# Optimization experiments

Hardware: AMD Instinct MI355X
Metric: run time of the kernel (lower is better)

Reference implementation:

```python
import jax, jax.numpy as jnp
import numpy as np

K = 9          # 3x3 deformable kernel positions
EPS = 1e-5     # BatchNorm eps


def conv3x3(x, w, stride=1):
    # x: [B,C,H,W], w: [O,I,3,3], padding=1
    return jax.lax.conv_general_dilated(
        x, w, (stride, stride), ((1, 1), (1, 1)),
        dimension_numbers=('NCHW', 'OIHW', 'NCHW'))


def _bilinear_sample(img, py, px):
    # img: [C,H,W]; py,px: [K,Ho,Wo] float sample coords (zero outside).
    H, W = img.shape[1], img.shape[2]
    y0 = jnp.floor(py)
    x0 = jnp.floor(px)

    def corner(yc, xc):
        w = (1.0 - jnp.abs(py - yc)) * (1.0 - jnp.abs(px - xc))
        valid = (yc >= 0) & (yc <= H - 1) & (xc >= 0) & (xc <= W - 1)
        yi = jnp.clip(yc, 0, H - 1).astype(jnp.int32)
        xi = jnp.clip(xc, 0, W - 1).astype(jnp.int32)
        v = img[:, yi, xi]                      # [C,K,Ho,Wo]
        return v * (w * valid)[None]

    return (corner(y0, x0) + corner(y0, x0 + 1) +
            corner(y0 + 1, x0) + corner(y0 + 1, x0 + 1))


def deform_conv2d(x, offset, mask, w, stride=1, pad=1):
    # x: [B,Cin,H,W]; offset: [B,2K,Ho,Wo] (y,x interleaved per tap);
    # mask: [B,K,Ho,Wo]; w: [Cout,Cin,3,3]. torchvision DCNv2 semantics.
    B, Cin = x.shape[0], x.shape[1]
    Ho, Wo = offset.shape[2], offset.shape[3]
    Cout = w.shape[0]
    kh, kw = jnp.meshgrid(jnp.arange(3), jnp.arange(3), indexing='ij')
    kh = kh.reshape(K).astype(x.dtype)
    kw = kw.reshape(K).astype(x.dtype)
    base_y = (jnp.arange(Ho) * stride - pad).astype(x.dtype)
    base_x = (jnp.arange(Wo) * stride - pad).astype(x.dtype)
    off = offset.reshape(B, K, 2, Ho, Wo)
    py = base_y[None, None, :, None] + kh[None, :, None, None] + off[:, :, 0]
    px = base_x[None, None, None, :] + kw[None, :, None, None] + off[:, :, 1]
    g = jax.vmap(_bilinear_sample)(x, py, px)     # [B,Cin,K,Ho,Wo]
    g = g * mask[:, None]
    return jnp.einsum('bikhw,oik->bohw', g, w.reshape(Cout, Cin, K))


def batchnorm(x, gamma, beta, mean, var):
    # eval-mode BN over channel dim of [B,C,H,W]
    inv = jax.lax.rsqrt(var + EPS) * gamma
    return x * inv[None, :, None, None] + (beta - mean * inv)[None, :, None, None]


def setup_inputs() -> dict:
    key = jax.random.key(0)
    ks = jax.random.split(key, 20)
    B, Cin, H, W = 16, 64, 64, 64
    C1, C2, NC = 128, 128, 1000
    inp = {
        'x': jax.random.normal(ks[0], (B, Cin, H, W), jnp.float32),
        'conv1_w': jax.random.normal(ks[1], (C1, Cin, 3, 3), jnp.float32) * 0.05,
        'off1_w': jax.random.normal(ks[2], (2 * K, Cin, 3, 3), jnp.float32) * 0.02,
        'mod1_w': jax.random.normal(ks[3], (K, Cin, 3, 3), jnp.float32) * 0.05,
        'bn1_g': jax.random.uniform(ks[4], (C1,), jnp.float32, 0.5, 1.5),
        'bn1_b': jax.random.normal(ks[5], (C1,), jnp.float32) * 0.1,
        'bn1_m': jax.random.normal(ks[6], (C1,), jnp.float32) * 0.1,
        'bn1_v': jax.random.uniform(ks[7], (C1,), jnp.float32, 0.5, 1.5),
        'conv2_w': jax.random.normal(ks[8], (C2, C1, 3, 3), jnp.float32) * 0.05,
        'off2_w': jax.random.normal(ks[9], (2 * K, C1, 3, 3), jnp.float32) * 0.02,
        'mod2_w': jax.random.normal(ks[10], (K, C1, 3, 3), jnp.float32) * 0.05,
        'bn2_g': jax.random.uniform(ks[11], (C2,), jnp.float32, 0.5, 1.5),
        'bn2_b': jax.random.normal(ks[12], (C2,), jnp.float32) * 0.1,
        'bn2_m': jax.random.normal(ks[13], (C2,), jnp.float32) * 0.1,
        'bn2_v': jax.random.uniform(ks[14], (C2,), jnp.float32, 0.5, 1.5),
        'fc_w': jax.random.normal(ks[15], (NC, C2), jnp.float32) * 0.05,
        'fc_b': jnp.zeros((NC,), jnp.float32),
    }
    return inp


def reference(x, conv1_w, off1_w, mod1_w, bn1_g, bn1_b, bn1_m, bn1_v,
              conv2_w, off2_w, mod2_w, bn2_g, bn2_b, bn2_m, bn2_v,
              fc_w, fc_b):
    stride = 1
    # stage 1: deformable conv (offset + sigmoid modulation) + BN + ReLU
    off = conv3x3(x, off1_w, stride)
    mask = jax.nn.sigmoid(conv3x3(x, mod1_w, stride))
    out = deform_conv2d(x, off, mask, conv1_w, stride=stride, pad=1)
    out = jax.nn.relu(batchnorm(out, bn1_g, bn1_b, bn1_m, bn1_v))
    # stage 2: deformable conv + BN (no ReLU before GAP, as in source)
    off = conv3x3(out, off2_w, stride)
    mask = jax.nn.sigmoid(conv3x3(out, mod2_w, stride))
    out = deform_conv2d(out, off, mask, conv2_w, stride=stride, pad=1)
    out = batchnorm(out, bn2_g, bn2_b, bn2_m, bn2_v)
    # global average pool + fc
    out = out.mean(axis=(2, 3))                 # [B, C2]
    return out @ fc_w.T + fc_b
```

## Files before the change

### kernel.cpp

```cpp
#include <hip/hip_runtime.h>

#define TPB 256
typedef unsigned short us;
typedef __attribute__((ext_vector_type(8))) _Float16 f16x8;
typedef __attribute__((ext_vector_type(2))) _Float16 f16x2;
typedef __attribute__((ext_vector_type(4))) float f32x4;

__device__ inline us f2h(float f){ union{ _Float16 h; us u; } x; x.h = (_Float16)f; return x.u; }
__device__ inline f16x2 u2h2(unsigned u){ union{ unsigned v; f16x2 h; } x; x.v = u; return x.h; }
#define MFMA16(a,b,c) __builtin_amdgcn_mfma_f32_16x16x32_f16((a),(b),(c),0,0,0)

__global__ __launch_bounds__(256) void k_transpose_x(const float* __restrict__ x,
                                                     us* __restrict__ xT){
  __shared__ float tile[64][65];
  const int y = blockIdx.x, b = blockIdx.y;
  for (int i = threadIdx.x; i < 4096; i += TPB){
    const int c = i >> 6, xx = i & 63;
    tile[c][xx] = x[b*262144 + c*4096 + y*64 + xx];
  }
  __syncthreads();
  for (int i = threadIdx.x; i < 4096; i += TPB){
    const int xx = i >> 6, c = i & 63;
    xT[(size_t)(b*4096 + y*64 + xx)*64 + c] = f2h(tile[c][xx]);
  }
}

__global__ __launch_bounds__(256) void k_prep(
    const float* __restrict__ cw1, const float* __restrict__ ow1, const float* __restrict__ mw1,
    const float* __restrict__ cw2, const float* __restrict__ ow2, const float* __restrict__ mw2,
    us* __restrict__ d1, us* __restrict__ d2, us* __restrict__ a1, us* __restrict__ a2){
  const int e = blockIdx.x*TPB + threadIdx.x;
  if (e < 73728){
    int k = e/8192, r = e%8192, kb = r/4096, r2 = r%4096;
    int n0 = r2>>9, q = r2&511, l = q>>3, j = q&7;
    int co = n0*16 + (l&15), c = kb*32 + (l>>4)*8 + j;
    d1[e] = f2h(cw1[(co*64 + c)*9 + k]);
  }
  if (e < 147456){
    int k = e/16384, r = e%16384, kb = r/4096, r2 = r%4096;
    int n0 = r2>>9, q = r2&511, l = q>>3, j = q&7;
    int co = n0*16 + (l&15), c = kb*32 + (l>>4)*8 + j;
    d2[e] = f2h(cw2[(co*128 + c)*9 + k]);
  }
  if (e < 18432){
    int k = e/2048, r = e%2048, kb = r/1024, r2 = r%1024;
    int n0 = r2>>9, q = r2&511, l = q>>3, j = q&7;
    int co = n0*16 + (l&15), c = kb*32 + (l>>4)*8 + j;
    float w = (co < 18) ? ow1[(co*64 + c)*9 + k] : (co < 27 ? mw1[((co-18)*64 + c)*9 + k] : 0.f);
    a1[e] = f2h(w);
  }
  if (e < 36864){
    int k = e/4096, r = e%4096, kb = r/1024, r2 = r%1024;
    int n0 = r2>>9, q = r2&511, l = q>>3, j = q&7;
    int co = n0*16 + (l&15), c = kb*32 + (l>>4)*8 + j;
    float w = (co < 18) ? ow2[(co*128 + c)*9 + k] : (co < 27 ? mw2[((co-18)*128 + c)*9 + k] : 0.f);
    a2[e] = f2h(w);
  }
}

template<int CIN, int STAGE>
__global__ __launch_bounds__(512, 4) void k_fused(
    const us* __restrict__ inT,
    const us* __restrict__ wb_aux, const us* __restrict__ wb_def,
    const float* __restrict__ bn_g, const float* __restrict__ bn_b,
    const float* __restrict__ bn_m, const float* __restrict__ bn_v,
    us* __restrict__ outT, float* __restrict__ partial){
  constexpr int KB2  = CIN/64;
  constexpr int NC   = 9*KB2;
  constexpr int WE_A = 2*(CIN/32)*512;
  constexpr int WE_D = 8*(CIN/32)*512;

  __shared__ __align__(16) us pool[12672];
  __shared__ uint4 otab[576];
  __shared__ uint2 wtab[576];
  __shared__ float extra[256];

  const int id  = blockIdx.x;
  const int nid = (id & 7)*128 + (id >> 3);
  const int b = nid >> 6, ho = nid & 63;
  const int tid = threadIdx.x;
  const us* __restrict__ inb = inT + (size_t)b*4096*CIN;
  const char* __restrict__ inbc = (const char*)inb;

  if (STAGE == 1 && tid < 128){
    float inv = rsqrtf(bn_v[tid] + 1e-5f)*bn_g[tid];
    extra[tid] = inv; extra[128 + tid] = bn_b[tid] - bn_m[tid]*inv;
  }

  const int lane = tid & 63, lr = lane & 15, lg = lane >> 4;
  const int wv = tid >> 6;

  const int mh = wv & 3, nh = wv >> 2;
  f32x4 aacc = (f32x4){0.f,0.f,0.f,0.f};
  for (int kb2 = 0; kb2 < KB2; ++kb2){
    if (kb2) __syncthreads();
    for (int s = tid; s < 1584; s += 512){
      const int slot = s >> 3, cq = s & 7;
      const int r = slot/66, p = slot - r*66;
      const int y = ho - 1 + r, x = p - 1;
      uint4 q = make_uint4(0u,0u,0u,0u);
      if (y >= 0 && y < 64 && x >= 0 && x < 64)
        q = *(const uint4*)(inb + (size_t)(y*64 + x)*CIN + kb2*64 + cq*8);
      *(uint4*)(pool + slot*64 + ((cq ^ (slot & 7))*8)) = q;
    }
    __syncthreads();
    #pragma unroll
    for (int k = 0; k < 9; ++k){
      const int kh = k/3, kw = k - kh*3;
      const int slot = kh*66 + mh*16 + lr + kw;
      #pragma unroll
      for (int kbl = 0; kbl < 2; ++kbl){
        f16x8 a = *(const f16x8*)(pool + slot*64 + (((kbl*4 + lg) ^ (slot & 7))*8));
        f16x8 bf = *(const f16x8*)(wb_aux + (size_t)k*WE_A + (size_t)((kb2*2 + kbl)*2 + nh)*512 + lane*8);
        aacc = MFMA16(a, bf, aacc);
      }
    }
  }
  __syncthreads();

  float* am = (float*)pool;
  {
    const int co = nh*16 + lr;
    if (co < 27){
      #pragma unroll
      for (int i = 0; i < 4; ++i) am[co*66 + mh*16 + lg*4 + i] = aacc[i];
    }
  }
  __syncthreads();

  for (int sid = tid; sid < 576; sid += 512){
    const int k = sid >> 6, px = sid & 63;
    const int kh = k/3, kw = k - kh*3;
    float oy = am[(2*k)*66 + px];
    float ox = am[(2*k+1)*66 + px];
    float mv = 1.f/(1.f + expf(-am[(18+k)*66 + px]));
    float py  = (float)(ho - 1 + kh) + oy;
    float pxx = (float)(px - 1 + kw) + ox;
    float fyf = floorf(py), fxf = floorf(pxx);
    int y0 = (int)fyf, x0 = (int)fxf;
    float dy = py - fyf, dx = pxx - fxf;
    bool vy0 = (y0 >= 0) && (y0 < 64), vy1 = (y0 >= -1) && (y0 < 63);
    bool vx0 = (x0 >= 0) && (x0 < 64), vx1 = (x0 >= -1) && (x0 < 63);
    int y0c = min(max(y0,0),63), y1c = min(max(y0+1,0),63);
    int x0c = min(max(x0,0),63), x1c = min(max(x0+1,0),63);
    const unsigned str = CIN*2u;
    otab[sid] = make_uint4((unsigned)(y0c*64 + x0c)*str, (unsigned)(y0c*64 + x1c)*str,
                           (unsigned)(y1c*64 + x0c)*str, (unsigned)(y1c*64 + x1c)*str);
    float w00 = (1.f-dy)*(1.f-dx)*mv*((vy0 && vx0) ? 1.f : 0.f);
    float w01 = (1.f-dy)*dx     *mv*((vy0 && vx1) ? 1.f : 0.f);
    float w10 = dy*(1.f-dx)     *mv*((vy1 && vx0) ? 1.f : 0.f);
    float w11 = dy*dx           *mv*((vy1 && vx1) ? 1.f : 0.f);
    wtab[sid] = make_uint2((unsigned)f2h(w00) | ((unsigned)f2h(w01) << 16),
                           (unsigned)f2h(w10) | ((unsigned)f2h(w11) << 16));
  }
  __syncthreads();

  f32x4 acc[4];
  #pragma unroll
  for (int m = 0; m < 4; ++m) acc[m] = (f32x4){0.f,0.f,0.f,0.f};

  const int pxs = tid >> 3, cqs = tid & 7;

  auto load_corners = [&](int i, f16x8* cr){
    const int k = i/KB2, kb2 = i - (i/KB2)*KB2;
    const uint4 o = otab[k*64 + pxs];
    const unsigned c0 = (unsigned)(kb2*64 + cqs*8)*2u;
    cr[0] = *(const f16x8*)(inbc + o.x + c0);
    cr[1] = *(const f16x8*)(inbc + o.y + c0);
    cr[2] = *(const f16x8*)(inbc + o.z + c0);
    cr[3] = *(const f16x8*)(inbc + o.w + c0);
  };
  auto load_B = [&](int i, f16x8* bbp){
    const int k = i/KB2, kb2 = i - (i/KB2)*KB2;
    #pragma unroll
    for (int kbl = 0; kbl < 2; ++kbl)
      bbp[kbl] = *(const f16x8*)(wb_def + (size_t)k*WE_D + (size_t)((kb2*2 + kbl)*8 + wv)*512 + lane*8);
  };
  auto blend_write = [&](int i, const f16x8* cr, us* dst){
    const int k = i/KB2;
    const uint2 wp = wtab[k*64 + pxs];
    const f16x2 wAB = u2h2(wp.x), wCD = u2h2(wp.y);
    const _Float16 wA = wAB[0], wB = wAB[1], wC = wCD[0], wD = wCD[1];
    const f16x8 va = (f16x8){wA,wA,wA,wA,wA,wA,wA,wA};
    const f16x8 vb = (f16x8){wB,wB,wB,wB,wB,wB,wB,wB};
    const f16x8 vc = (f16x8){wC,wC,wC,wC,wC,wC,wC,wC};
    const f16x8 vd = (f16x8){wD,wD,wD,wD,wD,wD,wD,wD};
    f16x8 r = cr[0]*va + cr[1]*vb;
    r = r + cr[2]*vc + cr[3]*vd;
    *(f16x8*)(dst + pxs*64 + ((cqs ^ (pxs & 7))*8)) = r;
  };
  auto mfma_def = [&](int i, const us* src, const f16x8* bbp){
    #pragma unroll
    for (int kbl = 0; kbl < 2; ++kbl){
      #pragma unroll
      for (int mt = 0; mt < 4; ++mt){
        const int row = mt*16 + lr;
        f16x8 a = *(const f16x8*)(src + row*64 + (((kbl*4 + lg) ^ (row & 7))*8));
        acc[mt] = MFMA16(a, bbp[kbl], acc[mt]);
      }
    }
  };

  us* g0 = pool;
  us* g1 = pool + 4096;
  f16x8 crn[4], bb[2], bbn[2];
  load_corners(0, crn);
  load_B(0, bb);
  blend_write(0, crn, g0);
  __syncthreads();
  for (int i = 0; i < NC; ++i){
    us* cur = (i & 1) ? g1 : g0;
    us* nxt = (i & 1) ? g0 : g1;
    const bool more = (i + 1 < NC);
    if (more){ load_corners(i+1, crn); load_B(i+1, bbn); }
    mfma_def(i, cur, bb);
    if (more) blend_write(i+1, crn, nxt);
    bb[0] = bbn[0]; bb[1] = bbn[1];
    __syncthreads();
  }

  if (STAGE == 1){
    const size_t rowbase = (size_t)(b*4096 + ho*64)*128;
    const int co = wv*16 + lr;
    const float inv = extra[co], bia = extra[128 + co];
    #pragma unroll
    for (int mt = 0; mt < 4; ++mt){
      const int pxl = mt*16 + lg*4;
      #pragma unroll
      for (int i = 0; i < 4; ++i){
        float v = acc[mt][i]*inv + bia;
        outT[rowbase + (size_t)(pxl + i)*128 + co] = f2h(fmaxf(v, 0.f));
      }
    }
  } else {
    float s = 0.f;
    #pragma unroll
    for (int mt = 0; mt < 4; ++mt)
      s += acc[mt][0] + acc[mt][1] + acc[mt][2] + acc[mt][3];
    s += __shfl_xor(s, 16);
    s += __shfl_xor(s, 32);
    if (lane < 16) extra[wv*16 + lane] = s;
    __syncthreads();
    if (tid < 128) partial[(size_t)(b*64 + ho)*128 + tid] = extra[tid];
  }
}

__global__ __launch_bounds__(256) void k_pool(
    const float* __restrict__ partial,
    const float* __restrict__ g2, const float* __restrict__ b2,
    const float* __restrict__ m2, const float* __restrict__ v2,
    float* __restrict__ pooled){
  const int t = blockIdx.x*TPB + threadIdx.x;
  if (t >= 2048) return;
  const int b = t >> 7, c = t & 127;
  float s = 0.f;
  for (int h = 0; h < 64; ++h) s += partial[(b*64 + h)*128 + c];
  const float inv = rsqrtf(v2[c] + 1e-5f)*g2[c];
  pooled[t] = s*(1.f/4096.f)*inv + (b2[c] - m2[c]*inv);
}

__global__ __launch_bounds__(256) void k_fc(
    const float* __restrict__ pooled, const float* __restrict__ fcw,
    const float* __restrict__ fcb, float* __restrict__ outp){
  const int t = blockIdx.x*TPB + threadIdx.x;
  if (t >= 16000) return;
  const int b = t/1000, n = t - b*1000;
  const float* p = pooled + b*128;
  const float* w = fcw + n*128;
  float s = fcb[n];
  #pragma unroll
  for (int c = 0; c < 128; c += 4){
    const float4 pv = *(const float4*)(p + c);
    const float4 wv = *(const float4*)(w + c);
    s = fmaf(pv.x, wv.x, s); s = fmaf(pv.y, wv.y, s);
    s = fmaf(pv.z, wv.z, s); s = fmaf(pv.w, wv.w, s);
  }
  outp[t] = s;
}

extern "C" void kernel_launch(void* const* d_in, const int* in_sizes, int n_in,
                              void* d_out, int out_size, void* d_ws, size_t ws_size,
                              hipStream_t stream){
  const float* x      = (const float*)d_in[0];
  const float* conv1w = (const float*)d_in[1];
  const float* off1w  = (const float*)d_in[2];
  const float* mod1w  = (const float*)d_in[3];
  const float* bn1g   = (const float*)d_in[4];
  const float* bn1b   = (const float*)d_in[5];
  const float* bn1m   = (const float*)d_in[6];
  const float* bn1v   = (const float*)d_in[7];
  const float* conv2w = (const float*)d_in[8];
  const float* off2w  = (const float*)d_in[9];
  const float* mod2w  = (const float*)d_in[10];
  const float* bn2g   = (const float*)d_in[11];
  const float* bn2b   = (const float*)d_in[12];
  const float* bn2m   = (const float*)d_in[13];
  const float* bn2v   = (const float*)d_in[14];
  const float* fcw    = (const float*)d_in[15];
  const float* fcb    = (const float*)d_in[16];

  char* w = (char*)d_ws;
  us*    xT      = (us*)(w);
  us*    out1T   = (us*)(w + 8388608);
  float* partial = (float*)(w + 25165824);
  float* pooled  = (float*)(w + 25690112);
  us*    wb_d1   = (us*)(w + 25698304);
  us*    wb_d2   = (us*)(w + 25845760);
  us*    wb_a1   = (us*)(w + 26140672);
  us*    wb_a2   = (us*)(w + 26177536);

  k_transpose_x<<<dim3(64,16), TPB, 0, stream>>>(x, xT);
  k_prep<<<576, TPB, 0, stream>>>(conv1w, off1w, mod1w, conv2w, off2w, mod2w,
                                  wb_d1, wb_d2, wb_a1, wb_a2);

  k_fused<64,1><<<1024, 512, 0, stream>>>(
      xT, wb_a1, wb_d1, bn1g, bn1b, bn1m, bn1v, out1T, nullptr);
  k_fused<128,2><<<1024, 512, 0, stream>>>(
      out1T, wb_a2, wb_d2, nullptr, nullptr, nullptr, nullptr, nullptr, partial);

  k_pool<<<8, TPB, 0, stream>>>(partial, bn2g, bn2b, bn2m, bn2v, pooled);
  k_fc<<<63, TPB, 0, stream>>>(pooled, fcw, fcb, (float*)d_out);
}
```

Before: 103.2 us.

## Deepen prefetch pipelining in offset-conv staging and deformable gather loop

```diff
diff --git a/kernel.cpp b/kernel.cpp
--- a/kernel.cpp
+++ b/kernel.cpp
@@ -89,21 +89,34 @@
 
   const int lane = tid & 63, lr = lane & 15, lg = lane >> 4;
   const int wv = tid >> 6;
-
   const int mh = wv & 3, nh = wv >> 2;
+
   f32x4 aacc = (f32x4){0.f,0.f,0.f,0.f};
-  for (int kb2 = 0; kb2 < KB2; ++kb2){
-    if (kb2) __syncthreads();
-    for (int s = tid; s < 1584; s += 512){
-      const int slot = s >> 3, cq = s & 7;
-      const int r = slot/66, p = slot - r*66;
-      const int y = ho - 1 + r, x = p - 1;
-      uint4 q = make_uint4(0u,0u,0u,0u);
-      if (y >= 0 && y < 64 && x >= 0 && x < 64)
-        q = *(const uint4*)(inb + (size_t)(y*64 + x)*CIN + kb2*64 + cq*8);
-      *(uint4*)(pool + slot*64 + ((cq ^ (slot & 7))*8)) = q;
-    }
-    __syncthreads();
+  auto load_rows = [&](int kb2, uint4* rq){
+    #pragma unroll
+    for (int it = 0; it < 4; ++it){
+      const int s = it*512 + tid;
+      if (s < 1584){
+        const int slot = s >> 3, cq = s & 7;
+        const int r = slot/66, p = slot - r*66;
+        const int y = ho - 1 + r, x = p - 1;
+        rq[it] = make_uint4(0u,0u,0u,0u);
+        if (y >= 0 && y < 64 && x >= 0 && x < 64)
+          rq[it] = *(const uint4*)(inb + (size_t)(y*64 + x)*CIN + kb2*64 + cq*8);
+      }
+    }
+  };
+  auto write_rows = [&](const uint4* rq){
+    #pragma unroll
+    for (int it = 0; it < 4; ++it){
+      const int s = it*512 + tid;
+      if (s < 1584){
+        const int slot = s >> 3, cq = s & 7;
+        *(uint4*)(pool + slot*64 + ((cq ^ (slot & 7))*8)) = rq[it];
+      }
+    }
+  };
+  auto mfma_aux = [&](int kb2){
     #pragma unroll
     for (int k = 0; k < 9; ++k){
       const int kh = k/3, kw = k - kh*3;
@@ -114,6 +127,20 @@
         f16x8 bf = *(const f16x8*)(wb_aux + (size_t)k*WE_A + (size_t)((kb2*2 + kbl)*2 + nh)*512 + lane*8);
         aacc = MFMA16(a, bf, aacc);
       }
+    }
+  };
+  {
+    uint4 rqA[4], rqB[4];
+    load_rows(0, rqA);
+    write_rows(rqA);
+    if constexpr (KB2 == 2) load_rows(1, rqB);
+    __syncthreads();
+    mfma_aux(0);
+    if constexpr (KB2 == 2){
+      __syncthreads();
+      write_rows(rqB);
+      __syncthreads();
+      mfma_aux(1);
     }
   }
   __syncthreads();
@@ -203,20 +230,24 @@
 
   us* g0 = pool;
   us* g1 = pool + 4096;
-  f16x8 crn[4], bb[2], bbn[2];
-  load_corners(0, crn);
-  load_B(0, bb);
-  blend_write(0, crn, g0);
-  __syncthreads();
-  for (int i = 0; i < NC; ++i){
-    us* cur = (i & 1) ? g1 : g0;
-    us* nxt = (i & 1) ? g0 : g1;
-    const bool more = (i + 1 < NC);
-    if (more){ load_corners(i+1, crn); load_B(i+1, bbn); }
-    mfma_def(i, cur, bb);
-    if (more) blend_write(i+1, crn, nxt);
-    bb[0] = bbn[0]; bb[1] = bbn[1];
+  f16x8 crA[4], crB[4], bbA[2], bbB[2];
+  load_corners(0, crA); load_B(0, bbA);
+  load_corners(1, crB); load_B(1, bbB);
+  blend_write(0, crA, g0);
+  __syncthreads();
+  for (int ii = 0; ii < NC; ii += 2){
+    if (ii + 2 < NC) load_corners(ii+2, crA);
+    mfma_def(ii, g0, bbA);
+    if (ii + 2 < NC) load_B(ii+2, bbA);
+    if (ii + 1 < NC) blend_write(ii+1, crB, g1);
     __syncthreads();
+    if (ii + 1 < NC){
+      if (ii + 3 < NC) load_corners(ii+3, crB);
+      mfma_def(ii+1, g1, bbB);
+      if (ii + 3 < NC) load_B(ii+3, bbB);
+      if (ii + 2 < NC) blend_write(ii+2, crA, g0);
+      __syncthreads();
+    }
   }
 
   if (STAGE == 1){
```

New measurement: 96.37 us. 1.07x faster.
